# Kernel tuning notes

Hardware: AMD Instinct MI355X
Metric: run time of the kernel (lower is better)

## Reference

```python
import jax, jax.numpy as jnp
from jax import lax
import numpy as np

# DP hyperparameters (from module __init__ defaults)
INS_DEL = 10.0
GAMMA = 1.0
FIRST_CHAR_COST = 10.0


def setup_inputs() -> dict:
    key = jax.random.key(0)
    k1, k2, k3 = jax.random.split(key, 3)
    B, T, M, V = 8192, 16, 16, 256
    tail_logits = jax.random.normal(k1, (B, T, V), dtype=jnp.float32)
    target_idx = jax.random.randint(k2, (B, M), 0, V, dtype=jnp.int32)
    c = jax.random.uniform(k3, (V, V), dtype=jnp.float32)
    # phonetic distance matrix: symmetric, zero diagonal (dist(a,a)=0)
    phon_cost = 0.5 * (c + c.T) * (1.0 - jnp.eye(V, dtype=jnp.float32))
    return {"tail_logits": tail_logits, "target_idx": target_idx, "phon_cost": phon_cost}


def _softmin3(a, b, c, gamma):
    # softmin(a,b,c) = -gamma * log(exp(-a/g)+exp(-b/g)+exp(-c/g))
    x = jnp.stack([a, b, c], axis=0)
    return -gamma * jax.nn.logsumexp(-x / gamma, axis=0)


def _rhyme_dp_loss(tail_logits, target_idx, phon_cost):
    # tail_logits: [B,T,V], target_idx: [B,M] int, phon_cost: [V,V]
    B, T, V = tail_logits.shape
    M = target_idx.shape[1]
    p = jax.nn.softmax(tail_logits, axis=-1)                      # [B,T,V]
    C_cols = phon_cost[:, target_idx]                             # [V,B,M]
    sub = jnp.einsum('btv,vbm->btm', p, C_cols)                   # expected sub cost [B,T,M]

    dt = sub.dtype
    row0 = jnp.broadcast_to(INS_DEL * jnp.arange(M + 1, dtype=dt), (B, M + 1))  # dp[0,:]
    left0s = INS_DEL * jnp.arange(1, T + 1, dtype=dt)             # dp[i,0], i=1..T

    def row_step(prev_row, xs):
        # prev_row: dp[i-1, :] -> [B, M+1]
        sub_i, left0 = xs                                         # sub_i: [B,M]
        init = jnp.full((B,), left0, dtype=dt)                    # dp[i,0]
        cells = (jnp.swapaxes(prev_row[:, 1:], 0, 1),             # up   dp[i-1,j]   [M,B]
                 jnp.swapaxes(prev_row[:, :-1], 0, 1),            # diag dp[i-1,j-1] [M,B]
                 jnp.swapaxes(sub_i, 0, 1))                       # sub[i-1,j-1]     [M,B]

        def cell(left, c):
            up, diag, s = c
            v = _softmin3(up + INS_DEL, left + INS_DEL, diag + s, GAMMA)
            return v, v

        _, vals = lax.scan(cell, init, cells)                     # vals: [M,B]
        row = jnp.concatenate([init[:, None], jnp.swapaxes(vals, 0, 1)], axis=1)
        return row, None

    final_row, _ = lax.scan(row_step, row0, (jnp.swapaxes(sub, 0, 1), left0s))
    dp_TM = final_row[:, -1]                                      # dp[T,M] per pair, [B]

    first_match_prob = jnp.take_along_axis(p[:, 0, :], target_idx[:, :1], axis=1)[:, 0]
    return dp_TM + FIRST_CHAR_COST * (1.0 - first_match_prob)     # [B]


def reference(tail_logits, target_idx, phon_cost):
    return _rhyme_dp_loss(tail_logits, target_idx, phon_cost)
```

## Files before the change

kernel.cpp:

```cpp
#include <hip/hip_runtime.h>

typedef __attribute__((ext_vector_type(8))) short short8;
typedef __attribute__((ext_vector_type(4))) float f32x4;

__device__ __forceinline__ short f2bf(float f) {
    unsigned u = __float_as_uint(f);
    u += 0x7fffu + ((u >> 16) & 1u);
    return (short)(u >> 16);
}

__global__ __launch_bounds__(256) void rhyme_dp_kernel(
    const float* __restrict__ logits,
    const int*   __restrict__ tidx,
    const float* __restrict__ phon,
    float*       __restrict__ out,
    int B)
{
    __shared__ float sub_lds[4][16][17];

    const int lane = threadIdx.x & 63;
    const int wv   = threadIdx.x >> 6;
    int b = blockIdx.x * 4 + wv;
    const bool valid = (b < B);
    if (!valid) b = 0;

    const int t = lane & 15;
    const int q = lane >> 4;

    const int idxn = tidx[b * 16 + t];
    const int idx0 = __shfl(idxn, 0);
    const int c0 = idx0 >> 5;
    const int q0 = (idx0 >> 3) & 3;
    const int j0 = idx0 & 7;

    const float* lp = logits + (size_t)b * 4096 + t * 256 + q * 8;
    const float* bp = phon   + (size_t)idxn * 256 + q * 8;

    f32x4 acc = {0.f, 0.f, 0.f, 0.f};
    float zsum = 0.f;
    float e0cap = 0.f;

    #pragma unroll
    for (int c = 0; c < 8; ++c) {
        const float4 x0 = *(const float4*)(lp + c * 32);
        const float4 x1 = *(const float4*)(lp + c * 32 + 4);
        const float4 y0 = *(const float4*)(bp + c * 32);
        const float4 y1 = *(const float4*)(bp + c * 32 + 4);

        const float e0_ = __expf(x0.x), e1_ = __expf(x0.y);
        const float e2_ = __expf(x0.z), e3_ = __expf(x0.w);
        const float e4_ = __expf(x1.x), e5_ = __expf(x1.y);
        const float e6_ = __expf(x1.z), e7_ = __expf(x1.w);
        zsum += ((e0_ + e1_) + (e2_ + e3_)) + ((e4_ + e5_) + (e6_ + e7_));

        if (c == c0) {
            const float a01 = (j0 & 1) ? e1_ : e0_;
            const float a23 = (j0 & 1) ? e3_ : e2_;
            const float a45 = (j0 & 1) ? e5_ : e4_;
            const float a67 = (j0 & 1) ? e7_ : e6_;
            const float b03 = (j0 & 2) ? a23 : a01;
            const float b47 = (j0 & 2) ? a67 : a45;
            const float sel = (j0 & 4) ? b47 : b03;
            if ((t == 0) && (q == q0)) e0cap = sel;
        }

        short8 af, bf;
        af[0] = f2bf(e0_); af[1] = f2bf(e1_); af[2] = f2bf(e2_); af[3] = f2bf(e3_);
        af[4] = f2bf(e4_); af[5] = f2bf(e5_); af[6] = f2bf(e6_); af[7] = f2bf(e7_);
        bf[0] = f2bf(y0.x); bf[1] = f2bf(y0.y); bf[2] = f2bf(y0.z); bf[3] = f2bf(y0.w);
        bf[4] = f2bf(y1.x); bf[5] = f2bf(y1.y); bf[6] = f2bf(y1.z); bf[7] = f2bf(y1.w);

        acc = __builtin_amdgcn_mfma_f32_16x16x32_bf16(af, bf, acc, 0, 0, 0);
    }

    zsum += __shfl_xor(zsum, 16);
    zsum += __shfl_xor(zsum, 32);
    const float rz = 1.0f / zsum;

    const float e0b = __shfl(e0cap, q0 * 16);
    const float rz0 = __shfl(rz, 0);
    const float p0  = e0b * rz0;

    #pragma unroll
    for (int r = 0; r < 4; ++r) {
        const float rzr = __shfl(rz, q * 4 + r);
        sub_lds[wv][q * 4 + r][t] = acc[r] * rzr;
    }
    __syncthreads();

    const int j = lane + 1;
    float P1 = 0.f, P2 = 0.f;
    for (int d = 2; d <= 32; ++d) {
        const int i = d - j;
        const float lnv = __shfl_up(P1, 1);
        const float dgv = __shfl_up(P2, 1);
        const float up   = (i == 1) ? 10.0f * (float)j : P1;
        const float left = (j == 1) ? 10.0f * (float)i : lnv;
        const float diag = (i == 1) ? 10.0f * (float)(j - 1)
                         : ((j == 1) ? 10.0f * (float)(i - 1) : dgv);
        int row = i - 1; row = row < 0 ? 0 : (row > 15 ? 15 : row);
        const float s  = sub_lds[wv][row][t];
        const float a  = up   + 10.0f;
        const float bb = left + 10.0f;
        const float cc = diag + s;
        const float mn = fminf(a, fminf(bb, cc));
        const float sm = __expf(mn - a) + __expf(mn - bb) + __expf(mn - cc);
        const float val = mn - __logf(sm);
        const bool act = (i >= 1) && (i <= 16);
        P2 = act ? P1 : P2;
        P1 = act ? val : P1;
    }

    if (valid && lane == 15) {
        out[b] = P1 + 10.0f * (1.0f - p0);
    }
}

extern "C" void kernel_launch(void* const* d_in, const int* in_sizes, int n_in,
                              void* d_out, int out_size, void* d_ws, size_t ws_size,
                              hipStream_t stream) {
    const float* logits = (const float*)d_in[0];
    const int*   tidx   = (const int*)d_in[1];
    const float* phon   = (const float*)d_in[2];
    float* out = (float*)d_out;

    const int B = in_sizes[0] / (16 * 256);
    const int blocks = (B + 3) / 4;
    hipLaunchKernelGGL(rhyme_dp_kernel, dim3(blocks), dim3(256), 0, stream,
                       logits, tidx, phon, out, B);
}
```

Measured before the change: 203.4 us.

## Prefetch logits into registers, pack bf16 via perm, run four DPs in one wave

All logits loads for a row are issued up front into a register array, so more memory requests are in flight before the exp and MFMA work starts. The per-element bf16 rounding is replaced by a packed add-and-perm conversion. That conversion rounds half up rather than to nearest even, a small numerical difference. The anti-diagonal DP is consolidated so wave 0 runs all four batch items' 16-lane DPs in parallel and the other waves exit early. This removes three waves' mostly idle serial DP work, at the cost of more register pressure from the prefetch.

```diff
diff --git a/kernel.cpp b/kernel.cpp
--- a/kernel.cpp
+++ b/kernel.cpp
@@ -2,11 +2,12 @@
 
 typedef __attribute__((ext_vector_type(8))) short short8;
 typedef __attribute__((ext_vector_type(4))) float f32x4;
+typedef __attribute__((ext_vector_type(4))) float vf4;
 
-__device__ __forceinline__ short f2bf(float f) {
-    unsigned u = __float_as_uint(f);
-    u += 0x7fffu + ((u >> 16) & 1u);
-    return (short)(u >> 16);
+__device__ __forceinline__ unsigned pk_bf16(float lo, float hi) {
+    const unsigned ul = __float_as_uint(lo) + 0x8000u;
+    const unsigned uh = __float_as_uint(hi) + 0x8000u;
+    return __builtin_amdgcn_perm(uh, ul, 0x07060302u);
 }
 
 __global__ __launch_bounds__(256) void rhyme_dp_kernel(
@@ -17,12 +18,12 @@
     int B)
 {
     __shared__ float sub_lds[4][16][17];
+    __shared__ float p0s[4];
 
     const int lane = threadIdx.x & 63;
     const int wv   = threadIdx.x >> 6;
     int b = blockIdx.x * 4 + wv;
-    const bool valid = (b < B);
-    if (!valid) b = 0;
+    if (b >= B) b = B - 1;
 
     const int t = lane & 15;
     const int q = lane >> 4;
@@ -36,21 +37,28 @@
     const float* lp = logits + (size_t)b * 4096 + t * 256 + q * 8;
     const float* bp = phon   + (size_t)idxn * 256 + q * 8;
 
+    vf4 xv[16];
+    #pragma unroll
+    for (int c = 0; c < 8; ++c) {
+        xv[2 * c]     = *(const vf4*)(lp + c * 32);
+        xv[2 * c + 1] = *(const vf4*)(lp + c * 32 + 4);
+    }
+
     f32x4 acc = {0.f, 0.f, 0.f, 0.f};
     float zsum = 0.f;
     float e0cap = 0.f;
 
     #pragma unroll
     for (int c = 0; c < 8; ++c) {
-        const float4 x0 = *(const float4*)(lp + c * 32);
-        const float4 x1 = *(const float4*)(lp + c * 32 + 4);
-        const float4 y0 = *(const float4*)(bp + c * 32);
-        const float4 y1 = *(const float4*)(bp + c * 32 + 4);
+        const vf4 x0 = xv[2 * c];
+        const vf4 x1 = xv[2 * c + 1];
+        const vf4 y0 = *(const vf4*)(bp + c * 32);
+        const vf4 y1 = *(const vf4*)(bp + c * 32 + 4);
 
-        const float e0_ = __expf(x0.x), e1_ = __expf(x0.y);
-        const float e2_ = __expf(x0.z), e3_ = __expf(x0.w);
-        const float e4_ = __expf(x1.x), e5_ = __expf(x1.y);
-        const float e6_ = __expf(x1.z), e7_ = __expf(x1.w);
+        const float e0_ = __expf(x0[0]), e1_ = __expf(x0[1]);
+        const float e2_ = __expf(x0[2]), e3_ = __expf(x0[3]);
+        const float e4_ = __expf(x1[0]), e5_ = __expf(x1[1]);
+        const float e6_ = __expf(x1[2]), e7_ = __expf(x1[3]);
         zsum += ((e0_ + e1_) + (e2_ + e3_)) + ((e4_ + e5_) + (e6_ + e7_));
 
         if (c == c0) {
@@ -64,13 +72,13 @@
             if ((t == 0) && (q == q0)) e0cap = sel;
         }
 
-        short8 af, bf;
-        af[0] = f2bf(e0_); af[1] = f2bf(e1_); af[2] = f2bf(e2_); af[3] = f2bf(e3_);
-        af[4] = f2bf(e4_); af[5] = f2bf(e5_); af[6] = f2bf(e6_); af[7] = f2bf(e7_);
-        bf[0] = f2bf(y0.x); bf[1] = f2bf(y0.y); bf[2] = f2bf(y0.z); bf[3] = f2bf(y0.w);
-        bf[4] = f2bf(y1.x); bf[5] = f2bf(y1.y); bf[6] = f2bf(y1.z); bf[7] = f2bf(y1.w);
+        union { short8 s; unsigned u[4]; } A, Bb;
+        A.u[0] = pk_bf16(e0_, e1_); A.u[1] = pk_bf16(e2_, e3_);
+        A.u[2] = pk_bf16(e4_, e5_); A.u[3] = pk_bf16(e6_, e7_);
+        Bb.u[0] = pk_bf16(y0[0], y0[1]); Bb.u[1] = pk_bf16(y0[2], y0[3]);
+        Bb.u[2] = pk_bf16(y1[0], y1[1]); Bb.u[3] = pk_bf16(y1[2], y1[3]);
 
-        acc = __builtin_amdgcn_mfma_f32_16x16x32_bf16(af, bf, acc, 0, 0, 0);
+        acc = __builtin_amdgcn_mfma_f32_16x16x32_bf16(A.s, Bb.s, acc, 0, 0, 0);
     }
 
     zsum += __shfl_xor(zsum, 16);
@@ -80,6 +88,7 @@
     const float e0b = __shfl(e0cap, q0 * 16);
     const float rz0 = __shfl(rz, 0);
     const float p0  = e0b * rz0;
+    if (lane == 0) p0s[wv] = p0;
 
     #pragma unroll
     for (int r = 0; r < 4; ++r) {
@@ -87,19 +96,23 @@
         sub_lds[wv][q * 4 + r][t] = acc[r] * rzr;
     }
     __syncthreads();
+    if (wv != 0) return;
 
-    const int j = lane + 1;
+    const int g  = lane >> 4;
+    const int tl = lane & 15;
+    const int j  = tl + 1;
     float P1 = 0.f, P2 = 0.f;
+    #pragma unroll
     for (int d = 2; d <= 32; ++d) {
-        const int i = d - j;
         const float lnv = __shfl_up(P1, 1);
         const float dgv = __shfl_up(P2, 1);
+        const int i = d - j;
         const float up   = (i == 1) ? 10.0f * (float)j : P1;
         const float left = (j == 1) ? 10.0f * (float)i : lnv;
         const float diag = (i == 1) ? 10.0f * (float)(j - 1)
                          : ((j == 1) ? 10.0f * (float)(i - 1) : dgv);
         int row = i - 1; row = row < 0 ? 0 : (row > 15 ? 15 : row);
-        const float s  = sub_lds[wv][row][t];
+        const float s  = sub_lds[g][row][tl];
         const float a  = up   + 10.0f;
         const float bb = left + 10.0f;
         const float cc = diag + s;
@@ -111,8 +124,9 @@
         P1 = act ? val : P1;
     }
 
-    if (valid && lane == 15) {
-        out[b] = P1 + 10.0f * (1.0f - p0);
+    const int gb = blockIdx.x * 4 + g;
+    if (tl == 15 && gb < B) {
+        out[gb] = P1 + 10.0f * (1.0f - p0s[g]);
     }
 }
 
```

Measured after the change: 195.7 us. 1.04x faster.
